# Kernel optimization log

Measured on AMD Instinct MI355X. Metric: run time of the kernel, lower is better.

## Reference

```python
import jax, jax.numpy as jnp
import numpy as np
import math

K_DIM = 1024
HEADS = 16

def setup_inputs() -> dict:
    key = jax.random.key(0)
    ks = jax.random.split(key, 6)
    b, N, k = 4, 2048, K_DIM
    sc = 1.0 / math.sqrt(k)
    return {
        "x": jax.random.normal(ks[0], (b, N, k), dtype=jnp.float32),
        "Wk": jax.random.normal(ks[1], (k, k), dtype=jnp.float32) * sc,
        "Wq": jax.random.normal(ks[2], (k, k), dtype=jnp.float32) * sc,
        "Wv": jax.random.normal(ks[3], (k, k), dtype=jnp.float32) * sc,
        "Wu": jax.random.normal(ks[4], (k, k), dtype=jnp.float32) * sc,
        "bu": jax.random.normal(ks[5], (k,), dtype=jnp.float32) * 0.01,
    }

def reference(x, Wk, Wq, Wv, Wu, bu):
    b, N, k = x.shape
    h = HEADS
    s = k // h
    # torch Linear: y = x @ W^T
    Q = (x @ Wq.T).reshape(b, N, h, s).transpose(0, 2, 1, 3)  # [b,h,N,s]
    Kh = (x @ Wk.T).reshape(b, N, h, s).transpose(0, 2, 1, 3)
    V = (x @ Wv.T).reshape(b, N, h, s).transpose(0, 2, 1, 3)
    scores = jnp.einsum('bhid,bhjd->bhij', Q, Kh) / math.sqrt(s)  # [b,h,N,N]
    attn = jax.nn.softmax(scores, axis=-1)
    out = jnp.einsum('bhij,bhjd->bhid', attn, V)  # [b,h,N,s]
    out = out.transpose(0, 2, 1, 3).reshape(b, N, k)
    return out @ Wu.T + bu
```

## Files before the change

### kernel.cpp

```cpp
#include <hip/hip_runtime.h>

typedef __bf16 bf16;
typedef __bf16 bf16x4 __attribute__((ext_vector_type(4)));
typedef __bf16 bf16x8 __attribute__((ext_vector_type(8)));
typedef float  f32x4  __attribute__((ext_vector_type(4)));

#define MFMA16(a, b, c) __builtin_amdgcn_mfma_f32_16x16x32_bf16((a), (b), (c), 0, 0, 0)

__device__ __forceinline__ void async_copy16(const void* g, void* l) {
  __builtin_amdgcn_global_load_lds(
      (const __attribute__((address_space(1))) unsigned int*)g,
      (__attribute__((address_space(3))) unsigned int*)l, 16, 0, 0);
}

struct CvtArgs {
  const float* src[5];
  bf16* dst[5];
  int blk_start[6];
};
__global__ void k_cvt_all(CvtArgs a) {
  int b = blockIdx.x;
  int seg = 0;
#pragma unroll
  for (int s = 1; s < 5; ++s) seg += (b >= a.blk_start[s]);
  int i = (b - a.blk_start[seg]) * 1024 + threadIdx.x * 4;
  float4 v = *(const float4*)(a.src[seg] + i);
  bf16x4 o = { (bf16)v.x, (bf16)v.y, (bf16)v.z, (bf16)v.w };
  *(bf16x4*)(a.dst[seg] + i) = o;
}

template <int OUTF32>
__device__ __forceinline__ void gemm128_body(
    const bf16* __restrict__ A, const bf16* __restrict__ B, void* __restrict__ Cp,
    const float* __restrict__ bias, int m0, int n0, int N, int K) {
  __shared__ alignas(16) bf16 As[128 * 32];
  __shared__ alignas(16) bf16 Bs[128 * 32];
  const int tid = threadIdx.x;
  const int lane = tid & 63;
  const int w = tid >> 6;
  const int quad = lane >> 4;
  const int l16 = lane & 15;
  const int wr = (w >> 1) * 64;
  const int wc = (w & 1) * 64;

  const int srow = tid >> 2;
  const int skk = (tid & 3) * 8;
  const bf16* Ag = A + (long)(m0 + srow) * K + skk;
  const bf16* Bg = B + (long)(n0 + srow) * K + skk;
  const long half = 64L * K;
  bf16* AsW = As + w * 512;
  bf16* BsW = Bs + w * 512;

  f32x4 acc[4][4];
#pragma unroll
  for (int i = 0; i < 4; ++i)
#pragma unroll
    for (int j = 0; j < 4; ++j) acc[i][j] = (f32x4){0.f, 0.f, 0.f, 0.f};

  for (int k0 = 0; k0 < K; k0 += 32) {
    async_copy16(Ag + k0, AsW);
    async_copy16(Ag + half + k0, AsW + 2048);
    async_copy16(Bg + k0, BsW);
    async_copy16(Bg + half + k0, BsW + 2048);
    __syncthreads();
    bf16x8 af[4], bfr[4];
#pragma unroll
    for (int i = 0; i < 4; ++i)
      af[i] = *(const bf16x8*)&As[(wr + i * 16 + l16) * 32 + quad * 8];
#pragma unroll
    for (int j = 0; j < 4; ++j)
      bfr[j] = *(const bf16x8*)&Bs[(wc + j * 16 + l16) * 32 + quad * 8];
#pragma unroll
    for (int i = 0; i < 4; ++i)
#pragma unroll
      for (int j = 0; j < 4; ++j) acc[i][j] = MFMA16(af[i], bfr[j], acc[i][j]);
    __syncthreads();
  }

#pragma unroll
  for (int i = 0; i < 4; ++i)
#pragma unroll
    for (int j = 0; j < 4; ++j)
#pragma unroll
      for (int r = 0; r < 4; ++r) {
        long row = m0 + wr + i * 16 + quad * 4 + r;
        int col = n0 + wc + j * 16 + l16;
        if (OUTF32)
          ((float*)Cp)[row * N + col] = acc[i][j][r] + bias[col];
        else
          ((bf16*)Cp)[row * N + col] = (bf16)acc[i][j][r];
      }
}

__global__ __launch_bounds__(256) void k_gemm_qkv(
    const bf16* __restrict__ xb, const bf16* __restrict__ Wqk, bf16* __restrict__ QKb,
    const bf16* __restrict__ Wvb, bf16* __restrict__ VtG) {
  int bid = blockIdx.x;
  if (bid < 1024) {
    int bm = bid & 63, bn = bid >> 6;
    gemm128_body<0>(xb, Wqk, QKb, nullptr, bm * 128, bn * 128, 2048, 1024);
  } else {
    int id = bid - 1024;
    int bm = id & 7, bn = id >> 3;
    gemm128_body<0>(Wvb, xb, VtG, nullptr, bm * 128, bn * 128, 8192, 1024);
  }
}

__global__ __launch_bounds__(256) void k_gemm_out(
    const bf16* __restrict__ Ab, const bf16* __restrict__ Wub, float* __restrict__ out,
    const float* __restrict__ bu) {
  gemm128_body<1>(Ab, Wub, out, bu, blockIdx.x * 128, blockIdx.y * 128, 1024, 1024);
}

__global__ __launch_bounds__(256, 2) void k_attn(
    const bf16* __restrict__ Q, const bf16* __restrict__ Kb,
    const bf16* __restrict__ Vt, bf16* __restrict__ O) {
  __shared__ alignas(16) bf16 Ps[256][72];
  __shared__ alignas(16) bf16 Ks[64][72];
  __shared__ alignas(16) bf16 Vs[64][72];

  const int tid = threadIdx.x;
  const int lane = tid & 63;
  const int w = tid >> 6;
  const int quad = lane >> 4;
  const int l16 = lane & 15;
  const int qt = blockIdx.x;
  const int bh = blockIdx.y;
  const int bb = bh >> 4;
  const int h = bh & 15;
  const int hoff = h * 64;
  const long rowQ0 = (long)bb * 2048 + qt * 256;
  const long kv0 = (long)bb * 2048;

  {
    const bf16* p = Q + (rowQ0 + tid) * 2048 + hoff;
#pragma unroll
    for (int u = 0; u < 8; ++u) {
      bf16x8 v = *(const bf16x8*)(p + u * 8);
      bf16x8 o;
#pragma unroll
      for (int j = 0; j < 8; ++j) o[j] = (bf16)((float)v[j] * 0.125f);
      *(bf16x8*)&Ps[tid][u * 8] = o;
    }
  }
  bf16x8 bq[4][2];
#pragma unroll
  for (int g = 0; g < 4; ++g)
#pragma unroll
    for (int ss = 0; ss < 2; ++ss)
      bq[g][ss] = *(const bf16x8*)&Ps[w * 64 + g * 16 + l16][ss * 32 + quad * 8];

  f32x4 accO[4][4];
  float lp[4] = {0.f, 0.f, 0.f, 0.f};
#pragma unroll
  for (int g = 0; g < 4; ++g)
#pragma unroll
    for (int t = 0; t < 4; ++t) accO[g][t] = (f32x4){0.f, 0.f, 0.f, 0.f};

  const int srow = tid >> 2;
  const int scol = (tid & 3) * 8;
  const bf16* kp = Kb + (kv0 + srow) * 2048 + hoff + scol;
  const bf16* vp = Vt + (long)(hoff + srow) * 8192 + kv0 + scol;

  bf16x8 kr0 = *(const bf16x8*)kp;
  bf16x8 kr1 = *(const bf16x8*)(kp + 32);
  bf16x8 vr0 = *(const bf16x8*)vp;
  bf16x8 vr1 = *(const bf16x8*)(vp + 32);

  for (int kt = 0; kt < 32; ++kt) {
    __syncthreads();
    *(bf16x8*)&Ks[srow][scol] = kr0;
    *(bf16x8*)&Ks[srow][scol + 32] = kr1;
    *(bf16x8*)&Vs[srow][scol] = vr0;
    *(bf16x8*)&Vs[srow][scol + 32] = vr1;
    __syncthreads();
    if (kt < 31) {
      const bf16* kp2 = kp + (long)(kt + 1) * 64 * 2048;
      const bf16* vp2 = vp + (kt + 1) * 64;
      kr0 = *(const bf16x8*)kp2;
      kr1 = *(const bf16x8*)(kp2 + 32);
      vr0 = *(const bf16x8*)vp2;
      vr1 = *(const bf16x8*)(vp2 + 32);
    }

    bf16x8 ak[4][2], bv[2][4];
#pragma unroll
    for (int mt = 0; mt < 4; ++mt) {
      ak[mt][0] = *(const bf16x8*)&Ks[mt * 16 + l16][quad * 8];
      ak[mt][1] = *(const bf16x8*)&Ks[mt * 16 + l16][32 + quad * 8];
    }
#pragma unroll
    for (int ss = 0; ss < 2; ++ss)
#pragma unroll
      for (int t = 0; t < 4; ++t)
        bv[ss][t] = *(const bf16x8*)&Vs[t * 16 + l16][ss * 32 + quad * 8];

#pragma unroll
    for (int g = 0; g < 4; ++g) {
      f32x4 st[4];
#pragma unroll
      for (int mt = 0; mt < 4; ++mt) {
        st[mt] = (f32x4){0.f, 0.f, 0.f, 0.f};
        st[mt] = MFMA16(ak[mt][0], bq[g][0], st[mt]);
        st[mt] = MFMA16(ak[mt][1], bq[g][1], st[mt]);
      }
#pragma unroll
      for (int mt = 0; mt < 4; ++mt) {
        bf16x4 pk;
#pragma unroll
        for (int r = 0; r < 4; ++r) {
          float pv = __expf(st[mt][r]);
          lp[g] += pv;
          pk[r] = (bf16)pv;
        }
        *(bf16x4*)&Ps[w * 64 + g * 16 + l16][mt * 16 + quad * 4] = pk;
      }
#pragma unroll
      for (int ss = 0; ss < 2; ++ss) {
        bf16x8 ap = *(const bf16x8*)&Ps[w * 64 + g * 16 + l16][ss * 32 + quad * 8];
#pragma unroll
        for (int t = 0; t < 4; ++t)
          accO[g][t] = MFMA16(ap, bv[ss][t], accO[g][t]);
      }
    }
  }

#pragma unroll
  for (int g = 0; g < 4; ++g) {
    float l = lp[g];
    l += __shfl_xor(l, 16);
    l += __shfl_xor(l, 32);
    float linv = 1.f / l;
#pragma unroll
    for (int r = 0; r < 4; ++r) {
      float inv = __shfl(linv, (lane & 48) | (quad * 4 + r));
      long row = rowQ0 + w * 64 + g * 16 + quad * 4 + r;
#pragma unroll
      for (int t = 0; t < 4; ++t)
        O[row * 1024 + hoff + t * 16 + l16] = (bf16)(accO[g][t][r] * inv);
    }
  }
}

extern "C" void kernel_launch(void* const* d_in, const int* in_sizes, int n_in,
                              void* d_out, int out_size, void* d_ws, size_t ws_size,
                              hipStream_t stream) {
  const float* x  = (const float*)d_in[0];
  const float* Wk = (const float*)d_in[1];
  const float* Wq = (const float*)d_in[2];
  const float* Wv = (const float*)d_in[3];
  const float* Wu = (const float*)d_in[4];
  const float* bu = (const float*)d_in[5];
  float* out = (float*)d_out;

  const int XE = 4 * 2048 * 1024;
  const int WE = 1024 * 1024;

  bf16* p = (bf16*)d_ws;
  bf16* xb   = p; p += XE;
  bf16* Wqkb = p; p += 2 * WE;
  bf16* Wvb  = p; p += WE;
  bf16* Wub  = p; p += WE;
  bf16* QKb  = p; p += 2 * XE;
  bf16* VtG  = p; p += XE;
  bf16* Ab   = p; p += XE;

  CvtArgs ca;
  ca.src[0] = x;  ca.dst[0] = xb;
  ca.src[1] = Wq; ca.dst[1] = Wqkb;
  ca.src[2] = Wk; ca.dst[2] = Wqkb + WE;
  ca.src[3] = Wv; ca.dst[3] = Wvb;
  ca.src[4] = Wu; ca.dst[4] = Wub;
  ca.blk_start[0] = 0;
  ca.blk_start[1] = XE / 1024;
  ca.blk_start[2] = ca.blk_start[1] + WE / 1024;
  ca.blk_start[3] = ca.blk_start[2] + WE / 1024;
  ca.blk_start[4] = ca.blk_start[3] + WE / 1024;
  ca.blk_start[5] = ca.blk_start[4] + WE / 1024;
  k_cvt_all<<<ca.blk_start[5], 256, 0, stream>>>(ca);

  k_gemm_qkv<<<1536, 256, 0, stream>>>(xb, Wqkb, QKb, Wvb, VtG);

  k_attn<<<dim3(8, 64), 256, 0, stream>>>(QKb, QKb + 1024, VtG, Ab);

  k_gemm_out<<<dim3(64, 8), 256, 0, stream>>>(Ab, Wub, out, bu);
}
```

Baseline: 265.2 us.

## Double-buffer attention K/V tiles, fold log2e into Q scale, reorder block mapping

The attention K/V shared tiles become double-buffered, so each iteration needs one barrier instead of two. The Q scale now includes log2(e), which lets the softmax use exp2 directly instead of __expf. The attention grid and the V-transpose GEMM block index mapping are swapped to change scheduling order and cache locality. Extra shared memory for the second buffer could reduce occupancy, and the score computation still never subtracts a running max, as before.

```diff
diff --git a/kernel.cpp b/kernel.cpp
--- a/kernel.cpp
+++ b/kernel.cpp
@@ -101,7 +101,7 @@
     gemm128_body<0>(xb, Wqk, QKb, nullptr, bm * 128, bn * 128, 2048, 1024);
   } else {
     int id = bid - 1024;
-    int bm = id & 7, bn = id >> 3;
+    int bn = id & 63, bm = id >> 6;
     gemm128_body<0>(Wvb, xb, VtG, nullptr, bm * 128, bn * 128, 8192, 1024);
   }
 }
@@ -116,16 +116,16 @@
     const bf16* __restrict__ Q, const bf16* __restrict__ Kb,
     const bf16* __restrict__ Vt, bf16* __restrict__ O) {
   __shared__ alignas(16) bf16 Ps[256][72];
-  __shared__ alignas(16) bf16 Ks[64][72];
-  __shared__ alignas(16) bf16 Vs[64][72];
+  __shared__ alignas(16) bf16 Ks[2][64][72];
+  __shared__ alignas(16) bf16 Vs[2][64][72];
 
   const int tid = threadIdx.x;
   const int lane = tid & 63;
   const int w = tid >> 6;
   const int quad = lane >> 4;
   const int l16 = lane & 15;
-  const int qt = blockIdx.x;
-  const int bh = blockIdx.y;
+  const int bh = blockIdx.x;
+  const int qt = blockIdx.y;
   const int bb = bh >> 4;
   const int h = bh & 15;
   const int hoff = h * 64;
@@ -134,12 +134,13 @@
 
   {
     const bf16* p = Q + (rowQ0 + tid) * 2048 + hoff;
+    const float qs = 0.18033688011112043f;
 #pragma unroll
     for (int u = 0; u < 8; ++u) {
       bf16x8 v = *(const bf16x8*)(p + u * 8);
       bf16x8 o;
 #pragma unroll
-      for (int j = 0; j < 8; ++j) o[j] = (bf16)((float)v[j] * 0.125f);
+      for (int j = 0; j < 8; ++j) o[j] = (bf16)((float)v[j] * qs);
       *(bf16x8*)&Ps[tid][u * 8] = o;
     }
   }
@@ -168,12 +169,12 @@
   bf16x8 vr1 = *(const bf16x8*)(vp + 32);
 
   for (int kt = 0; kt < 32; ++kt) {
-    __syncthreads();
-    *(bf16x8*)&Ks[srow][scol] = kr0;
-    *(bf16x8*)&Ks[srow][scol + 32] = kr1;
-    *(bf16x8*)&Vs[srow][scol] = vr0;
-    *(bf16x8*)&Vs[srow][scol + 32] = vr1;
-    __syncthreads();
+    bf16 (*kbuf)[72] = Ks[kt & 1];
+    bf16 (*vbuf)[72] = Vs[kt & 1];
+    *(bf16x8*)&kbuf[srow][scol] = kr0;
+    *(bf16x8*)&kbuf[srow][scol + 32] = kr1;
+    *(bf16x8*)&vbuf[srow][scol] = vr0;
+    *(bf16x8*)&vbuf[srow][scol + 32] = vr1;
     if (kt < 31) {
       const bf16* kp2 = kp + (long)(kt + 1) * 64 * 2048;
       const bf16* vp2 = vp + (kt + 1) * 64;
@@ -182,18 +183,19 @@
       vr0 = *(const bf16x8*)vp2;
       vr1 = *(const bf16x8*)(vp2 + 32);
     }
+    __syncthreads();
 
     bf16x8 ak[4][2], bv[2][4];
 #pragma unroll
     for (int mt = 0; mt < 4; ++mt) {
-      ak[mt][0] = *(const bf16x8*)&Ks[mt * 16 + l16][quad * 8];
-      ak[mt][1] = *(const bf16x8*)&Ks[mt * 16 + l16][32 + quad * 8];
+      ak[mt][0] = *(const bf16x8*)&kbuf[mt * 16 + l16][quad * 8];
+      ak[mt][1] = *(const bf16x8*)&kbuf[mt * 16 + l16][32 + quad * 8];
     }
 #pragma unroll
     for (int ss = 0; ss < 2; ++ss)
 #pragma unroll
       for (int t = 0; t < 4; ++t)
-        bv[ss][t] = *(const bf16x8*)&Vs[t * 16 + l16][ss * 32 + quad * 8];
+        bv[ss][t] = *(const bf16x8*)&vbuf[t * 16 + l16][ss * 32 + quad * 8];
 
 #pragma unroll
     for (int g = 0; g < 4; ++g) {
@@ -209,7 +211,7 @@
         bf16x4 pk;
 #pragma unroll
         for (int r = 0; r < 4; ++r) {
-          float pv = __expf(st[mt][r]);
+          float pv = __builtin_exp2f(st[mt][r]);
           lp[g] += pv;
           pk[r] = (bf16)pv;
         }
@@ -281,7 +283,7 @@
 
   k_gemm_qkv<<<1536, 256, 0, stream>>>(xb, Wqkb, QKb, Wvb, VtG);
 
-  k_attn<<<dim3(8, 64), 256, 0, stream>>>(QKb, QKb + 1024, VtG, Ab);
+  k_attn<<<dim3(64, 8), 256, 0, stream>>>(QKb, QKb + 1024, VtG, Ab);
 
   k_gemm_out<<<dim3(64, 8), 256, 0, stream>>>(Ab, Wub, out, bu);
 }
```

Measured after the change: 305.0 us. 15.0% more time.
